# Performance work log

Measured on AMD Instinct MI355X. Metric: run time of the kernel, lower is better.

Reference implementation:

```python
import jax, jax.numpy as jnp
import numpy as np

D_MODEL = 1024
NUM_LAYERS = 4
VOCAB = 32000
NUM_HEADS = 8
HEAD_DIM = D_MODEL // NUM_HEADS
FFN_DIM = 2048
BATCH = 4
SEQ = 1024
LN_EPS = 1e-5
ROPE_THETA = 10000.0


def setup_inputs() -> dict:
    key = jax.random.key(0)
    ks = iter(jax.random.split(key, 32))
    std = 0.02
    L, D, H, Dh, F, V = NUM_LAYERS, D_MODEL, NUM_HEADS, HEAD_DIM, FFN_DIM, VOCAB
    inp = {
        "tokens": jax.random.randint(next(ks), (BATCH, SEQ), 0, V, dtype=jnp.int32),
        "emb": jax.random.normal(next(ks), (V, D), jnp.float32),
        # per-layer stacked params; Linear weights stored pre-transposed (in, out)
        "Wqkv": jax.random.normal(next(ks), (L, D, 3 * D), jnp.float32) * std,
        "bqkv": jnp.zeros((L, 3 * D), jnp.float32),
        "Wo": jax.random.normal(next(ks), (L, D, D), jnp.float32) * std,
        "bo": jnp.zeros((L, D), jnp.float32),
        "ln1_g": jnp.ones((L, D), jnp.float32),
        "ln1_b": jnp.zeros((L, D), jnp.float32),
        "ln2_g": jnp.ones((L, D), jnp.float32),
        "ln2_b": jnp.zeros((L, D), jnp.float32),
        "W1": jax.random.normal(next(ks), (L, D, F), jnp.float32) * std,
        "b1": jnp.zeros((L, F), jnp.float32),
        "W2": jax.random.normal(next(ks), (L, F, D), jnp.float32) * std,
        "b2": jnp.zeros((L, D), jnp.float32),
        "lnf_g": jnp.ones((D,), jnp.float32),
        "lnf_b": jnp.zeros((D,), jnp.float32),
        "Wout": jax.random.normal(next(ks), (D, V), jnp.float32) * std,
        "bout": jnp.zeros((V,), jnp.float32),
    }
    return inp


def _layernorm(x, g, b):
    mu = jnp.mean(x, -1, keepdims=True)
    var = jnp.mean(jnp.square(x - mu), -1, keepdims=True)
    return (x - mu) * jax.lax.rsqrt(var + LN_EPS) * g + b


def _rope_cos_sin(seq, dh, dtype):
    inv_freq = 1.0 / (ROPE_THETA ** (jnp.arange(0, dh, 2, dtype=jnp.float32) / dh))
    t = jnp.arange(seq, dtype=jnp.float32)
    freqs = jnp.outer(t, inv_freq)                      # [S, Dh/2]
    emb = jnp.concatenate([freqs, freqs], axis=-1)      # [S, Dh]
    return jnp.cos(emb).astype(dtype), jnp.sin(emb).astype(dtype)


def _rotate_half(x):
    x1, x2 = jnp.split(x, 2, axis=-1)
    return jnp.concatenate([-x2, x1], axis=-1)


def _apply_rope(x, cos, sin):
    # x: [B,S,H,Dh]; cos/sin: [S,Dh] -> broadcast over batch and heads
    return x * cos[None, :, None, :] + _rotate_half(x) * sin[None, :, None, :]


def reference(tokens, emb, Wqkv, bqkv, Wo, bo, ln1_g, ln1_b, ln2_g, ln2_b,
              W1, b1, W2, b2, lnf_g, lnf_b, Wout, bout):
    B, S = tokens.shape
    H, Dh = NUM_HEADS, HEAD_DIM
    x = emb[tokens]                                      # [B,S,D]
    cos, sin = _rope_cos_sin(S, Dh, x.dtype)
    causal = jnp.tril(jnp.ones((S, S), dtype=bool))      # True = keep
    scale = 1.0 / jnp.sqrt(jnp.asarray(Dh, x.dtype))

    def layer(xc, p):
        (wqkv, bq, wo, bo_, g1, b1_, g2, b2_, w1, bb1, w2, bb2) = p
        y = _layernorm(xc, g1, b1_)
        qkv = (y @ wqkv + bq).reshape(B, S, 3, H, Dh)
        q, k, v = qkv[:, :, 0], qkv[:, :, 1], qkv[:, :, 2]
        q = _apply_rope(q, cos, sin)
        k = _apply_rope(k, cos, sin)
        scores = jnp.einsum("bshd,bthd->bhst", q, k) * scale
        scores = jnp.where(causal[None, None], scores, -jnp.inf)
        attn = jax.nn.softmax(scores, axis=-1)
        ctx = jnp.einsum("bhst,bthd->bshd", attn, v).reshape(B, S, H * Dh)
        xc = xc + ctx @ wo + bo_
        z = _layernorm(xc, g2, b2_)
        ff = jax.nn.gelu(z @ w1 + bb1, approximate=False) @ w2 + bb2
        return xc + ff, None

    params = (Wqkv, bqkv, Wo, bo, ln1_g, ln1_b, ln2_g, ln2_b, W1, b1, W2, b2)
    x, _ = jax.lax.scan(layer, x, params)
    x = _layernorm(x, lnf_g, lnf_b)
    return x @ Wout + bout                                # [B,S,V]
```

## Files before the change

### kernel.cpp

```cpp
#include <hip/hip_runtime.h>
#include <hip/hip_bf16.h>
#include <math.h>


#define D_MODEL 1024
#define SEQ     1024
#define BATCH   4
#define NHEAD   8
#define HDIM    128
#define FFN     2048
#define NLAYER  4
#define VOCAB   32000
#define MROWS   (BATCH*SEQ)

typedef unsigned short ushort_t;
typedef __attribute__((ext_vector_type(8))) short s16x8;
typedef __attribute__((ext_vector_type(4))) float f32x4;

__device__ __forceinline__ ushort_t f2bf(float f) {
    union { float f; unsigned int u; } c; c.f = f;
    unsigned int u = c.u;
    unsigned int r = (u + 0x7FFFu + ((u >> 16) & 1u)) >> 16;
    return (ushort_t)r;
}
__device__ __forceinline__ float bf2f(ushort_t u) {
    union { unsigned int u; float f; } c; c.u = ((unsigned int)u) << 16; return c.f;
}

__device__ __forceinline__ void gload16(const void* g, void* l) {
    __builtin_amdgcn_global_load_lds(
        (const __attribute__((address_space(1))) unsigned int*)g,
        (__attribute__((address_space(3))) unsigned int*)l, 16, 0, 0);
}

__global__ __launch_bounds__(256) void embed_kernel(
    const int* __restrict__ tokens, const float* __restrict__ emb,
    float* __restrict__ X)
{
    int row = blockIdx.x;
    int t = tokens[row];
    const float4* src = (const float4*)(emb + (size_t)t * D_MODEL);
    float4* dst = (float4*)(X + (size_t)row * D_MODEL);
    dst[threadIdx.x] = src[threadIdx.x];
}

__global__ __launch_bounds__(256) void ln_kernel(
    const float* __restrict__ X, const float* __restrict__ g,
    const float* __restrict__ b, ushort_t* __restrict__ Y)
{
    __shared__ float red[8];
    int row = blockIdx.x;
    const float4* x4 = (const float4*)(X + (size_t)row * D_MODEL);
    float4 v = x4[threadIdx.x];
    float s  = v.x + v.y + v.z + v.w;
    float ss = v.x*v.x + v.y*v.y + v.z*v.z + v.w*v.w;
    #pragma unroll
    for (int o = 32; o > 0; o >>= 1) { s += __shfl_down(s, o); ss += __shfl_down(ss, o); }
    int wid = threadIdx.x >> 6;
    if ((threadIdx.x & 63) == 0) { red[wid] = s; red[wid + 4] = ss; }
    __syncthreads();
    float tot  = red[0] + red[1] + red[2] + red[3];
    float tot2 = red[4] + red[5] + red[6] + red[7];
    float mu  = tot * (1.0f / D_MODEL);
    float var = tot2 * (1.0f / D_MODEL) - mu * mu;
    float r = rsqrtf(var + 1e-5f);
    const float4* g4 = (const float4*)g;
    const float4* b4 = (const float4*)b;
    float4 gv = g4[threadIdx.x], bv = b4[threadIdx.x];
    ushort4 o;
    o.x = f2bf((v.x - mu) * r * gv.x + bv.x);
    o.y = f2bf((v.y - mu) * r * gv.y + bv.y);
    o.z = f2bf((v.z - mu) * r * gv.z + bv.z);
    o.w = f2bf((v.w - mu) * r * gv.w + bv.w);
    ((ushort4*)(Y + (size_t)row * D_MODEL))[threadIdx.x] = o;
}

__global__ __launch_bounds__(256) void wconv(
    const float* __restrict__ W, ushort_t* __restrict__ Wt, int K, int N)
{
    __shared__ float t[32][33];
    const float* Wl = W + (size_t)blockIdx.z * K * N;
    ushort_t* Wtl = Wt + (size_t)blockIdx.z * K * N;
    int k0 = blockIdx.y * 32, n0 = blockIdx.x * 32;
    int tid = threadIdx.x;
    int r = tid >> 3, c4 = (tid & 7) * 4;
    float4 v = *(const float4*)(Wl + (size_t)(k0 + r) * N + n0 + c4);
    t[r][c4+0] = v.x; t[r][c4+1] = v.y; t[r][c4+2] = v.z; t[r][c4+3] = v.w;
    __syncthreads();
    ushort4 o;
    o.x = f2bf(t[c4+0][r]); o.y = f2bf(t[c4+1][r]);
    o.z = f2bf(t[c4+2][r]); o.w = f2bf(t[c4+3][r]);
    *(ushort4*)(Wtl + (size_t)(n0 + r) * K + k0 + c4) = o;
}

__device__ __forceinline__ float gelu_exact(float x) {
    return 0.5f * x * (1.0f + erff(x * 0.70710678118654752f));
}

template<int ACT, int BETA, int OBF>
__global__ __launch_bounds__(256) void gemm_mfma(
    const ushort_t* __restrict__ A, const ushort_t* __restrict__ Bt,
    const float* __restrict__ bias, float* __restrict__ Cf,
    ushort_t* __restrict__ Cb, int M, int N, int K)
{
    __shared__ __align__(16) ushort_t As[128 * 32];
    __shared__ __align__(16) ushort_t Bs[128 * 32];
    int tid  = threadIdx.x;
    int lane = tid & 63, w = tid >> 6;
    int wr = w >> 1, wc = w & 1;
    int m0 = blockIdx.x * 128, n0 = blockIdx.y * 128;

    f32x4 acc[4][4] = {};

    const ushort_t* gA = A  + (size_t)(m0 + w * 32 + (lane >> 2)) * K + (lane & 3) * 8;
    const ushort_t* gB = Bt + (size_t)(n0 + w * 32 + (lane >> 2)) * K + (lane & 3) * 8;
    ushort_t* lA = As + w * 1024;
    ushort_t* lB = Bs + w * 1024;
    const size_t gstep16 = (size_t)16 * K;

    int lrow = lane & 15, kg = lane >> 4;
    const s16x8* pa = (const s16x8*)(As + (wr * 64 + lrow) * 32 + kg * 8);
    const s16x8* pb = (const s16x8*)(Bs + (wc * 64 + lrow) * 32 + kg * 8);

    for (int kt = 0; kt < K / 32; ++kt) {
        gload16(gA, lA);
        gload16(gA + gstep16, lA + 512);
        gload16(gB, lB);
        gload16(gB + gstep16, lB + 512);
        gA += 32; gB += 32;
        __syncthreads();
        s16x8 a[4], b[4];
        #pragma unroll
        for (int mi = 0; mi < 4; ++mi) a[mi] = pa[mi * 64];
        #pragma unroll
        for (int ni = 0; ni < 4; ++ni) b[ni] = pb[ni * 64];
        #pragma unroll
        for (int mi = 0; mi < 4; ++mi)
            #pragma unroll
            for (int ni = 0; ni < 4; ++ni)
                acc[mi][ni] = __builtin_amdgcn_mfma_f32_16x16x32_bf16(
                    a[mi], b[ni], acc[mi][ni], 0, 0, 0);
        __syncthreads();
    }

    #pragma unroll
    for (int mi = 0; mi < 4; ++mi) {
        int rbase = m0 + wr * 64 + mi * 16 + (lane >> 4) * 4;
        #pragma unroll
        for (int ni = 0; ni < 4; ++ni) {
            int col = n0 + wc * 64 + ni * 16 + (lane & 15);
            float bz = bias[col];
            f32x4 v = acc[mi][ni];
            #pragma unroll
            for (int j = 0; j < 4; ++j) {
                float x = v[j] + bz;
                if (ACT == 1) x = gelu_exact(x);
                size_t off = (size_t)(rbase + j) * N + col;
                if (OBF) {
                    Cb[off] = f2bf(x);
                } else {
                    if (BETA) x += Cf[off];
                    Cf[off] = x;
                }
            }
        }
    }
}

__global__ __launch_bounds__(512) void gemm_big(
    const ushort_t* __restrict__ A, const ushort_t* __restrict__ Bt,
    const float* __restrict__ bias, float* __restrict__ C,
    int M, int N, int K)
{
    __shared__ __align__(16) ushort_t As[2][256 * 64];
    __shared__ __align__(16) ushort_t Bs[2][256 * 64];
    int tid = threadIdx.x, lane = tid & 63, w = tid >> 6;
    int wm = w >> 2, wn = w & 3;
    int m0 = blockIdx.x * 256, n0 = blockIdx.y * 256;
    int lr = lane & 15, kg = lane >> 4;
    const int NKT = K / 64;

    f32x4 acc[8][4] = {};

    int srow = w * 8 + (lane >> 3);
    int scol = (((lane & 7) ^ ((lane >> 3) & 7))) * 8;

    int rsw = lr & 7;
    int ch0 = (kg    ) ^ rsw;
    int ch1 = (kg + 4) ^ rsw;

#define STAGE_A(db, ht, ktile) do { \
    const ushort_t* s_ = A + (size_t)(m0 + (ht) * 128 + srow) * K + (size_t)(ktile) * 64 + scol; \
    gload16(s_,                  &As[db][((ht) * 128 + w * 8) * 64]); \
    gload16(s_ + (size_t)64 * K, &As[db][((ht) * 128 + 64 + w * 8) * 64]); \
} while (0)
#define STAGE_B(db, ht, ktile) do { \
    const ushort_t* s_ = Bt + (size_t)(n0 + (ht) * 128 + srow) * K + (size_t)(ktile) * 64 + scol; \
    gload16(s_,                  &Bs[db][((ht) * 128 + w * 8) * 64]); \
    gload16(s_ + (size_t)64 * K, &Bs[db][((ht) * 128 + 64 + w * 8) * 64]); \
} while (0)
#define SBAR() do { __builtin_amdgcn_sched_barrier(0); \
    __builtin_amdgcn_s_barrier(); __builtin_amdgcn_sched_barrier(0); } while (0)

    STAGE_A(0, 0, 0); STAGE_A(0, 1, 0); STAGE_B(0, 0, 0); STAGE_B(0, 1, 0);
    STAGE_A(1, 0, 1);
    asm volatile("s_waitcnt vmcnt(2)" ::: "memory");
    SBAR();

    for (int kt = 0; kt < NKT; ++kt) {
        int d = kt & 1, dn = d ^ 1;
        const ushort_t* pa0 = &As[d][(wm * 128 + lr) * 64 + ch0 * 8];
        const ushort_t* pa1 = &As[d][(wm * 128 + lr) * 64 + ch1 * 8];
        const ushort_t* pb0 = &Bs[d][(wn * 64  + lr) * 64 + ch0 * 8];
        const ushort_t* pb1 = &Bs[d][(wn * 64  + lr) * 64 + ch1 * 8];
        s16x8 a03[4][2], a47[4][2], b01[2][2], b23[2][2];

        #pragma unroll
        for (int mi = 0; mi < 4; ++mi) {
            a03[mi][0] = *(const s16x8*)(pa0 + mi * 1024);
            a03[mi][1] = *(const s16x8*)(pa1 + mi * 1024);
        }
        #pragma unroll
        for (int ni = 0; ni < 2; ++ni) {
            b01[ni][0] = *(const s16x8*)(pb0 + ni * 1024);
            b01[ni][1] = *(const s16x8*)(pb1 + ni * 1024);
        }
        #pragma unroll
        for (int ni = 0; ni < 2; ++ni) {
            b23[ni][0] = *(const s16x8*)(pb0 + (2 + ni) * 1024);
            b23[ni][1] = *(const s16x8*)(pb1 + (2 + ni) * 1024);
        }
        #pragma unroll
        for (int mi = 0; mi < 4; ++mi) {
            a47[mi][0] = *(const s16x8*)(pa0 + (4 + mi) * 1024);
            a47[mi][1] = *(const s16x8*)(pa1 + (4 + mi) * 1024);
        }
        if (kt + 1 < NKT) STAGE_A(dn, 1, kt + 1);
        __builtin_amdgcn_sched_barrier(0);

        __builtin_amdgcn_s_setprio(1);
        #pragma unroll
        for (int mi = 0; mi < 4; ++mi)
            #pragma unroll
            for (int ni = 0; ni < 2; ++ni)
                #pragma unroll
                for (int kk = 0; kk < 2; ++kk)
                    acc[mi][ni] = __builtin_amdgcn_mfma_f32_16x16x32_bf16(
                        a03[mi][kk], b01[ni][kk], acc[mi][ni], 0, 0, 0);
        __builtin_amdgcn_s_setprio(0);
        __builtin_amdgcn_sched_barrier(0);
        if (kt + 1 < NKT) STAGE_B(dn, 0, kt + 1);
        __builtin_amdgcn_sched_barrier(0);

        __builtin_amdgcn_s_setprio(1);
        #pragma unroll
        for (int mi = 0; mi < 4; ++mi)
            #pragma unroll
            for (int ni = 0; ni < 2; ++ni)
                #pragma unroll
                for (int kk = 0; kk < 2; ++kk)
                    acc[mi][2 + ni] = __builtin_amdgcn_mfma_f32_16x16x32_bf16(
                        a03[mi][kk], b23[ni][kk], acc[mi][2 + ni], 0, 0, 0);
        __builtin_amdgcn_s_setprio(0);
        __builtin_amdgcn_sched_barrier(0);
        if (kt + 1 < NKT) STAGE_B(dn, 1, kt + 1);
        __builtin_amdgcn_sched_barrier(0);

        __builtin_amdgcn_s_setprio(1);
        #pragma unroll
        for (int mi = 0; mi < 4; ++mi)
            #pragma unroll
            for (int ni = 0; ni < 2; ++ni)
                #pragma unroll
                for (int kk = 0; kk < 2; ++kk)
                    acc[4 + mi][ni] = __builtin_amdgcn_mfma_f32_16x16x32_bf16(
                        a47[mi][kk], b01[ni][kk], acc[4 + mi][ni], 0, 0, 0);
        __builtin_amdgcn_s_setprio(0);

        asm volatile("s_waitcnt lgkmcnt(0)" ::: "memory");
        SBAR();
        if (kt + 2 < NKT) STAGE_A(d, 0, kt + 2);
        __builtin_amdgcn_sched_barrier(0);

        __builtin_amdgcn_s_setprio(1);
        #pragma unroll
        for (int mi = 0; mi < 4; ++mi)
            #pragma unroll
            for (int ni = 0; ni < 2; ++ni)
                #pragma unroll
                for (int kk = 0; kk < 2; ++kk)
                    acc[4 + mi][2 + ni] = __builtin_amdgcn_mfma_f32_16x16x32_bf16(
                        a47[mi][kk], b23[ni][kk], acc[4 + mi][2 + ni], 0, 0, 0);
        __builtin_amdgcn_s_setprio(0);

        if (kt + 2 < NKT) {
            asm volatile("s_waitcnt vmcnt(2)" ::: "memory");
        } else {
            asm volatile("s_waitcnt vmcnt(0)" ::: "memory");
        }
        SBAR();
    }
#undef STAGE_A
#undef STAGE_B
#undef SBAR

    #pragma unroll
    for (int mi = 0; mi < 8; ++mi) {
        int rbase = m0 + wm * 128 + mi * 16 + kg * 4;
        #pragma unroll
        for (int ni = 0; ni < 4; ++ni) {
            int col = n0 + wn * 64 + ni * 16 + lr;
            float bz = bias[col];
            f32x4 v = acc[mi][ni];
            #pragma unroll
            for (int j = 0; j < 4; ++j)
                C[(size_t)(rbase + j) * N + col] = v[j] + bz;
        }
    }
}

__global__ __launch_bounds__(64) void rope_table_kernel(float2* __restrict__ RT)
{
    int s = blockIdx.x, p = threadIdx.x;
    float inv = expf(-0.14391156831212788f * (float)p);
    float ang = (float)s * inv;
    float sn, c;
    sincosf(ang, &sn, &c);
    RT[s * 64 + p] = make_float2(c, sn);
}

__global__ __launch_bounds__(256) void ropeq_kernel(
    const ushort_t* __restrict__ QKVb, const float2* __restrict__ RT,
    ushort_t* __restrict__ Qb, ushort_t* __restrict__ Kb)
{
    int m = blockIdx.x;
    int b = m >> 10, s = m & (SEQ - 1);
    const ushort_t* rowbase = QKVb + (size_t)m * (3 * D_MODEL);
    const float2* t2 = RT + s * 64;
    int tid = threadIdx.x;
    int qk = tid >> 7;
    int rem = tid & 127;
    int hh = rem >> 4;
    int p4 = (rem & 15) * 4;
    const ushort_t* base = rowbase + qk * D_MODEL + hh * HDIM + p4;
    ushort4 lo = *(const ushort4*)base;
    ushort4 hi = *(const ushort4*)(base + 64);
    ushort_t lov[4] = {lo.x, lo.y, lo.z, lo.w};
    ushort_t hiv[4] = {hi.x, hi.y, hi.z, hi.w};
    ushort_t lor[4], hir[4];
    #pragma unroll
    for (int j = 0; j < 4; ++j) {
        float2 cs = t2[p4 + j];
        float x1 = bf2f(lov[j]), x2 = bf2f(hiv[j]);
        lor[j] = f2bf(x1 * cs.x - x2 * cs.y);
        hir[j] = f2bf(x2 * cs.x + x1 * cs.y);
    }
    ushort_t* dst = (qk ? Kb : Qb) + ((size_t)(b * NHEAD + hh) * SEQ + s) * HDIM + p4;
    *(ushort4*)dst        = make_ushort4(lor[0], lor[1], lor[2], lor[3]);
    *(ushort4*)(dst + 64) = make_ushort4(hir[0], hir[1], hir[2], hir[3]);
}

__global__ __launch_bounds__(256) void vtrans_kernel(
    const ushort_t* __restrict__ QKVb, ushort_t* __restrict__ Vt)
{
    __shared__ ushort_t tl[64][34];
    int s0 = blockIdx.x * 64;
    int d0 = blockIdx.y * 32;
    int b  = blockIdx.z;
    int tid = threadIdx.x;
    #pragma unroll
    for (int r = 0; r < 4; ++r) {
        int li = tid + r * 256;
        int row = li >> 4;
        int cp  = (li & 15) * 2;
        ushort2 v = *(const ushort2*)(QKVb + (size_t)(b * SEQ + s0 + row) * 3072
                                      + 2 * D_MODEL + d0 + cp);
        tl[row][cp]     = v.x;
        tl[row][cp + 1] = v.y;
    }
    __syncthreads();
    #pragma unroll
    for (int r = 0; r < 4; ++r) {
        int li = tid + r * 256;
        int drow = li >> 5;
        int sc   = (li & 31) * 2;
        ushort2 o;
        o.x = tl[sc][drow];
        o.y = tl[sc + 1][drow];
        *(ushort2*)(Vt + (size_t)(b * D_MODEL + d0 + drow) * SEQ + s0 + sc) = o;
    }
}

#define PSTR 72

__global__ __launch_bounds__(256) void attn_mfma(
    const ushort_t* __restrict__ Qb, const ushort_t* __restrict__ Kb,
    const ushort_t* __restrict__ Vt, ushort_t* __restrict__ Yb)
{
    __shared__ __align__(16) ushort_t Ks[64 * 136];
    __shared__ __align__(16) ushort_t Vts[128 * 72];
    __shared__ __align__(16) ushort_t Pl[4][16 * PSTR];
    int bid = blockIdx.x;
    int qt = bid & 15, h = (bid >> 4) & 7, b = bid >> 7;
    int q0 = qt * 64;
    int tid = threadIdx.x, lane = tid & 63, w = tid >> 6;
    int lr = lane & 15, g = lane >> 4;
    const float scale = 0.08838834764831845f;

    const ushort_t* Qbase = Qb + (size_t)((b * NHEAD + h) * SEQ) * HDIM;
    const ushort_t* Kbase = Kb + (size_t)((b * NHEAD + h) * SEQ) * HDIM;
    const ushort_t* Vbase = Vt + (size_t)(b * D_MODEL + h * HDIM) * SEQ;

    s16x8 aq[4];
    #pragma unroll
    for (int kc = 0; kc < 4; ++kc)
        aq[kc] = *(const s16x8*)(Qbase + (size_t)(q0 + w * 16 + lr) * HDIM + kc * 32 + g * 8);

    f32x4 acc_o[8] = {};
    float mx[4] = {-INFINITY, -INFINITY, -INFINITY, -INFINITY};
    float ls[4] = {};

    int ntiles = q0 / 64 + 1;
    for (int t = 0; t < ntiles; ++t) {
        int j0 = t * 64;
        __syncthreads();
        #pragma unroll
        for (int r = 0; r < 4; ++r) {
            int idx = tid + r * 256;
            int row = idx >> 4, c16 = idx & 15;
            *(s16x8*)&Ks[row * 136 + c16 * 8] =
                *(const s16x8*)(Kbase + (size_t)(j0 + row) * HDIM + c16 * 8);
        }
        #pragma unroll
        for (int r = 0; r < 4; ++r) {
            int idx = tid + r * 256;
            int row = idx >> 3, c8 = idx & 7;
            *(s16x8*)&Vts[row * 72 + c8 * 8] =
                *(const s16x8*)(Vbase + (size_t)row * SEQ + j0 + c8 * 8);
        }
        __syncthreads();

        f32x4 sa[4] = {};
        __builtin_amdgcn_s_setprio(1);
        #pragma unroll
        for (int nb = 0; nb < 4; ++nb)
            #pragma unroll
            for (int kc = 0; kc < 4; ++kc) {
                s16x8 bk = *(const s16x8*)&Ks[(nb * 16 + lr) * 136 + kc * 32 + g * 8];
                sa[nb] = __builtin_amdgcn_mfma_f32_16x16x32_bf16(aq[kc], bk, sa[nb], 0, 0, 0);
            }
        __builtin_amdgcn_s_setprio(0);

        bool diag = (j0 == q0);
        float pv[4][4];
        #pragma unroll
        for (int nb = 0; nb < 4; ++nb)
            #pragma unroll
            for (int j = 0; j < 4; ++j) {
                float v = sa[nb][j] * scale;
                if (diag) {
                    int kv = j0 + nb * 16 + lr;
                    int qq = q0 + w * 16 + g * 4 + j;
                    if (kv > qq) v = -INFINITY;
                }
                pv[nb][j] = v;
            }
        #pragma unroll
        for (int j = 0; j < 4; ++j) {
            float tm = fmaxf(fmaxf(pv[0][j], pv[1][j]), fmaxf(pv[2][j], pv[3][j]));
            #pragma unroll
            for (int o = 1; o < 16; o <<= 1) tm = fmaxf(tm, __shfl_xor(tm, o));
            float nm = fmaxf(mx[j], tm);
            float corr = expf(mx[j] - nm);
            float ts = 0.0f;
            #pragma unroll
            for (int nb = 0; nb < 4; ++nb) {
                float e = expf(pv[nb][j] - nm);
                pv[nb][j] = e;
                ts += e;
            }
            #pragma unroll
            for (int o = 1; o < 16; o <<= 1) ts += __shfl_xor(ts, o);
            ls[j] = ls[j] * corr + ts;
            mx[j] = nm;
            #pragma unroll
            for (int dn = 0; dn < 8; ++dn) acc_o[dn][j] *= corr;
        }
        #pragma unroll
        for (int nb = 0; nb < 4; ++nb)
            #pragma unroll
            for (int j = 0; j < 4; ++j)
                Pl[w][(g * 4 + j) * PSTR + nb * 16 + lr] = f2bf(pv[nb][j]);
        #pragma unroll
        for (int kk = 0; kk < 2; ++kk) {
            s16x8 pa = *(const s16x8*)&Pl[w][lr * PSTR + kk * 32 + g * 8];
            __builtin_amdgcn_s_setprio(1);
            #pragma unroll
            for (int dn = 0; dn < 8; ++dn) {
                s16x8 bv = *(const s16x8*)&Vts[(dn * 16 + lr) * 72 + kk * 32 + g * 8];
                acc_o[dn] = __builtin_amdgcn_mfma_f32_16x16x32_bf16(pa, bv, acc_o[dn], 0, 0, 0);
            }
            __builtin_amdgcn_s_setprio(0);
        }
    }

    float il[4];
    #pragma unroll
    for (int j = 0; j < 4; ++j) il[j] = 1.0f / ls[j];
    #pragma unroll
    for (int dn = 0; dn < 8; ++dn)
        #pragma unroll
        for (int j = 0; j < 4; ++j) {
            int q = q0 + w * 16 + g * 4 + j;
            Yb[(size_t)(b * SEQ + q) * D_MODEL + h * HDIM + dn * 16 + lr] =
                f2bf(acc_o[dn][j] * il[j]);
        }
}

extern "C" void kernel_launch(void* const* d_in, const int* in_sizes, int n_in,
                              void* d_out, int out_size, void* d_ws, size_t ws_size,
                              hipStream_t stream)
{
    const int*   tokens = (const int*)  d_in[0];
    const float* emb    = (const float*)d_in[1];
    const float* Wqkv   = (const float*)d_in[2];
    const float* bqkv   = (const float*)d_in[3];
    const float* Wo     = (const float*)d_in[4];
    const float* bo     = (const float*)d_in[5];
    const float* ln1_g  = (const float*)d_in[6];
    const float* ln1_b  = (const float*)d_in[7];
    const float* ln2_g  = (const float*)d_in[8];
    const float* ln2_b  = (const float*)d_in[9];
    const float* W1     = (const float*)d_in[10];
    const float* b1     = (const float*)d_in[11];
    const float* W2     = (const float*)d_in[12];
    const float* b2     = (const float*)d_in[13];
    const float* lnf_g  = (const float*)d_in[14];
    const float* lnf_b  = (const float*)d_in[15];
    const float* Wout   = (const float*)d_in[16];
    const float* bout   = (const float*)d_in[17];
    float* out = (float*)d_out;

    char* ws = (char*)d_ws;
    float*    X      = (float*)ws;
    ushort_t* Abuf   = (ushort_t*)(ws + 16777216);
    ushort_t* QKVb   = (ushort_t*)(ws + 25165824);
    ushort_t* Gbuf   = (ushort_t*)(ws + 25165824);
    ushort_t* Qbb    = (ushort_t*)(ws + 50331648);
    ushort_t* Kbb    = (ushort_t*)(ws + 58720256);
    ushort_t* Vtb    = (ushort_t*)(ws + 67108864);
    ushort_t* WqkvT  = (ushort_t*)(ws + 75497472);
    ushort_t* WoT    = (ushort_t*)(ws + 100663296);
    ushort_t* W1T    = (ushort_t*)(ws + 109051904);
    ushort_t* W2T    = (ushort_t*)(ws + 125829120);
    ushort_t* WoutT  = (ushort_t*)(ws + 142606336);
    float2*   RT     = (float2*)  (ws + 208142336);

    const int M = MROWS, Dm = D_MODEL, F = FFN, V = VOCAB;

    rope_table_kernel<<<SEQ, 64, 0, stream>>>(RT);

    wconv<<<dim3(3*Dm/32, Dm/32, NLAYER), 256, 0, stream>>>(Wqkv, WqkvT, Dm, 3*Dm);
    wconv<<<dim3(Dm/32,   Dm/32, NLAYER), 256, 0, stream>>>(Wo,   WoT,   Dm, Dm);
    wconv<<<dim3(F/32,    Dm/32, NLAYER), 256, 0, stream>>>(W1,   W1T,   Dm, F);
    wconv<<<dim3(Dm/32,   F/32,  NLAYER), 256, 0, stream>>>(W2,   W2T,   F,  Dm);
    wconv<<<dim3(V/32,    Dm/32, 1),      256, 0, stream>>>(Wout, WoutT, Dm, V);

    embed_kernel<<<MROWS, 256, 0, stream>>>(tokens, emb, X);

    for (int L = 0; L < NLAYER; ++L) {
        ln_kernel<<<MROWS, 256, 0, stream>>>(X, ln1_g + (size_t)L*Dm, ln1_b + (size_t)L*Dm, Abuf);
        gemm_mfma<0,0,1><<<dim3(M/128, 3*Dm/128), 256, 0, stream>>>(
            Abuf, WqkvT + (size_t)L*3*Dm*Dm, bqkv + (size_t)L*3*Dm, nullptr, QKVb, M, 3*Dm, Dm);
        ropeq_kernel<<<MROWS, 256, 0, stream>>>(QKVb, RT, Qbb, Kbb);
        vtrans_kernel<<<dim3(SEQ/64, Dm/32, BATCH), 256, 0, stream>>>(QKVb, Vtb);
        attn_mfma<<<BATCH*NHEAD*(SEQ/64), 256, 0, stream>>>(Qbb, Kbb, Vtb, Abuf);
        gemm_mfma<0,1,0><<<dim3(M/128, Dm/128), 256, 0, stream>>>(
            Abuf, WoT + (size_t)L*Dm*Dm, bo + (size_t)L*Dm, X, nullptr, M, Dm, Dm);
        ln_kernel<<<MROWS, 256, 0, stream>>>(X, ln2_g + (size_t)L*Dm, ln2_b + (size_t)L*Dm, Abuf);
        gemm_mfma<1,0,1><<<dim3(M/128, F/128), 256, 0, stream>>>(
            Abuf, W1T + (size_t)L*Dm*F, b1 + (size_t)L*F, nullptr, Gbuf, M, F, Dm);
        gemm_mfma<0,1,0><<<dim3(M/128, Dm/128), 256, 0, stream>>>(
            Gbuf, W2T + (size_t)L*F*Dm, b2 + (size_t)L*Dm, X, nullptr, M, Dm, F);
    }

    ln_kernel<<<MROWS, 256, 0, stream>>>(X, lnf_g, lnf_b, Abuf);
    gemm_big<<<dim3(M/256, V/256), 512, 0, stream>>>(
        Abuf, WoutT, bout, out, M, V, Dm);
}
```

Baseline: 1.516 ms.

## Double-buffer layer GEMMs with K=64 tiles, XOR-swizzled LDS and interleaved prefetch

```diff
diff --git a/kernel.cpp b/kernel.cpp
--- a/kernel.cpp
+++ b/kernel.cpp
@@ -31,6 +31,10 @@
     __builtin_amdgcn_global_load_lds(
         (const __attribute__((address_space(1))) unsigned int*)g,
         (__attribute__((address_space(3))) unsigned int*)l, 16, 0, 0);
+}
+
+__device__ __forceinline__ float gelu_exact(float x) {
+    return 0.5f * x * (1.0f + erff(x * 0.70710678118654752f));
 }
 
 __global__ __launch_bounds__(256) void embed_kernel(
@@ -93,62 +97,140 @@
     *(ushort4*)(Wtl + (size_t)(n0 + r) * K + k0 + c4) = o;
 }
 
-__device__ __forceinline__ float gelu_exact(float x) {
-    return 0.5f * x * (1.0f + erff(x * 0.70710678118654752f));
-}
-
 template<int ACT, int BETA, int OBF>
-__global__ __launch_bounds__(256) void gemm_mfma(
+__global__ __launch_bounds__(256) void gemm_mid(
     const ushort_t* __restrict__ A, const ushort_t* __restrict__ Bt,
     const float* __restrict__ bias, float* __restrict__ Cf,
     ushort_t* __restrict__ Cb, int M, int N, int K)
 {
-    __shared__ __align__(16) ushort_t As[128 * 32];
-    __shared__ __align__(16) ushort_t Bs[128 * 32];
-    int tid  = threadIdx.x;
-    int lane = tid & 63, w = tid >> 6;
-    int wr = w >> 1, wc = w & 1;
+    __shared__ __align__(16) ushort_t As[2][128 * 64];
+    __shared__ __align__(16) ushort_t Bs[2][128 * 64];
+    int tid = threadIdx.x, lane = tid & 63, w = tid >> 6;
+    int wm = w >> 1, wn = w & 1;
     int m0 = blockIdx.x * 128, n0 = blockIdx.y * 128;
+    int lr = lane & 15, kg = lane >> 4;
+    const int NKT = K / 64;
 
     f32x4 acc[4][4] = {};
 
-    const ushort_t* gA = A  + (size_t)(m0 + w * 32 + (lane >> 2)) * K + (lane & 3) * 8;
-    const ushort_t* gB = Bt + (size_t)(n0 + w * 32 + (lane >> 2)) * K + (lane & 3) * 8;
-    ushort_t* lA = As + w * 1024;
-    ushort_t* lB = Bs + w * 1024;
-    const size_t gstep16 = (size_t)16 * K;
-
-    int lrow = lane & 15, kg = lane >> 4;
-    const s16x8* pa = (const s16x8*)(As + (wr * 64 + lrow) * 32 + kg * 8);
-    const s16x8* pb = (const s16x8*)(Bs + (wc * 64 + lrow) * 32 + kg * 8);
-
-    for (int kt = 0; kt < K / 32; ++kt) {
-        gload16(gA, lA);
-        gload16(gA + gstep16, lA + 512);
-        gload16(gB, lB);
-        gload16(gB + gstep16, lB + 512);
-        gA += 32; gB += 32;
-        __syncthreads();
-        s16x8 a[4], b[4];
-        #pragma unroll
-        for (int mi = 0; mi < 4; ++mi) a[mi] = pa[mi * 64];
-        #pragma unroll
-        for (int ni = 0; ni < 4; ++ni) b[ni] = pb[ni * 64];
-        #pragma unroll
-        for (int mi = 0; mi < 4; ++mi)
-            #pragma unroll
-            for (int ni = 0; ni < 4; ++ni)
-                acc[mi][ni] = __builtin_amdgcn_mfma_f32_16x16x32_bf16(
-                    a[mi], b[ni], acc[mi][ni], 0, 0, 0);
-        __syncthreads();
-    }
+    int srow = w * 8 + (lane >> 3);
+    int scol = (((lane & 7) ^ ((lane >> 3) & 7))) * 8;
+
+    int rsw = lr & 7;
+    int ch0 = (kg    ) ^ rsw;
+    int ch1 = (kg + 4) ^ rsw;
+
+#define STAGE_A(db, ht, ktile) do { \
+    const ushort_t* s_ = A + (size_t)(m0 + (ht) * 64 + srow) * K + (size_t)(ktile) * 64 + scol; \
+    gload16(s_,                  &As[db][((ht) * 64 + w * 8) * 64]); \
+    gload16(s_ + (size_t)32 * K, &As[db][((ht) * 64 + 32 + w * 8) * 64]); \
+} while (0)
+#define STAGE_B(db, ht, ktile) do { \
+    const ushort_t* s_ = Bt + (size_t)(n0 + (ht) * 64 + srow) * K + (size_t)(ktile) * 64 + scol; \
+    gload16(s_,                  &Bs[db][((ht) * 64 + w * 8) * 64]); \
+    gload16(s_ + (size_t)32 * K, &Bs[db][((ht) * 64 + 32 + w * 8) * 64]); \
+} while (0)
+#define SBAR() do { __builtin_amdgcn_sched_barrier(0); \
+    __builtin_amdgcn_s_barrier(); __builtin_amdgcn_sched_barrier(0); } while (0)
+
+    STAGE_A(0, 0, 0); STAGE_A(0, 1, 0); STAGE_B(0, 0, 0); STAGE_B(0, 1, 0);
+    STAGE_A(1, 0, 1);
+    asm volatile("s_waitcnt vmcnt(2)" ::: "memory");
+    SBAR();
+
+    for (int kt = 0; kt < NKT; ++kt) {
+        int d = kt & 1, dn = d ^ 1;
+        const ushort_t* pa0 = &As[d][(wm * 64 + lr) * 64 + ch0 * 8];
+        const ushort_t* pa1 = &As[d][(wm * 64 + lr) * 64 + ch1 * 8];
+        const ushort_t* pb0 = &Bs[d][(wn * 64 + lr) * 64 + ch0 * 8];
+        const ushort_t* pb1 = &Bs[d][(wn * 64 + lr) * 64 + ch1 * 8];
+        s16x8 a[4][2], b[4][2];
+
+        #pragma unroll
+        for (int mi = 0; mi < 4; ++mi) {
+            a[mi][0] = *(const s16x8*)(pa0 + mi * 1024);
+            a[mi][1] = *(const s16x8*)(pa1 + mi * 1024);
+        }
+        #pragma unroll
+        for (int ni = 0; ni < 4; ++ni) {
+            b[ni][0] = *(const s16x8*)(pb0 + ni * 1024);
+            b[ni][1] = *(const s16x8*)(pb1 + ni * 1024);
+        }
+        if (kt + 1 < NKT) STAGE_A(dn, 1, kt + 1);
+        __builtin_amdgcn_sched_barrier(0);
+
+        __builtin_amdgcn_s_setprio(1);
+        #pragma unroll
+        for (int mi = 0; mi < 2; ++mi)
+            #pragma unroll
+            for (int ni = 0; ni < 2; ++ni)
+                #pragma unroll
+                for (int kk = 0; kk < 2; ++kk)
+                    acc[mi][ni] = __builtin_amdgcn_mfma_f32_16x16x32_bf16(
+                        a[mi][kk], b[ni][kk], acc[mi][ni], 0, 0, 0);
+        __builtin_amdgcn_s_setprio(0);
+        __builtin_amdgcn_sched_barrier(0);
+        if (kt + 1 < NKT) STAGE_B(dn, 0, kt + 1);
+        __builtin_amdgcn_sched_barrier(0);
+
+        __builtin_amdgcn_s_setprio(1);
+        #pragma unroll
+        for (int mi = 0; mi < 2; ++mi)
+            #pragma unroll
+            for (int ni = 2; ni < 4; ++ni)
+                #pragma unroll
+                for (int kk = 0; kk < 2; ++kk)
+                    acc[mi][ni] = __builtin_amdgcn_mfma_f32_16x16x32_bf16(
+                        a[mi][kk], b[ni][kk], acc[mi][ni], 0, 0, 0);
+        __builtin_amdgcn_s_setprio(0);
+        __builtin_amdgcn_sched_barrier(0);
+        if (kt + 1 < NKT) STAGE_B(dn, 1, kt + 1);
+        __builtin_amdgcn_sched_barrier(0);
+
+        __builtin_amdgcn_s_setprio(1);
+        #pragma unroll
+        for (int mi = 2; mi < 4; ++mi)
+            #pragma unroll
+            for (int ni = 0; ni < 2; ++ni)
+                #pragma unroll
+                for (int kk = 0; kk < 2; ++kk)
+                    acc[mi][ni] = __builtin_amdgcn_mfma_f32_16x16x32_bf16(
+                        a[mi][kk], b[ni][kk], acc[mi][ni], 0, 0, 0);
+        __builtin_amdgcn_s_setprio(0);
+
+        asm volatile("s_waitcnt lgkmcnt(0)" ::: "memory");
+        SBAR();
+        if (kt + 2 < NKT) STAGE_A(d, 0, kt + 2);
+        __builtin_amdgcn_sched_barrier(0);
+
+        __builtin_amdgcn_s_setprio(1);
+        #pragma unroll
+        for (int mi = 2; mi < 4; ++mi)
+            #pragma unroll
+            for (int ni = 2; ni < 4; ++ni)
+                #pragma unroll
+                for (int kk = 0; kk < 2; ++kk)
+                    acc[mi][ni] = __builtin_amdgcn_mfma_f32_16x16x32_bf16(
+                        a[mi][kk], b[ni][kk], acc[mi][ni], 0, 0, 0);
+        __builtin_amdgcn_s_setprio(0);
+
+        if (kt + 2 < NKT) {
+            asm volatile("s_waitcnt vmcnt(2)" ::: "memory");
+        } else {
+            asm volatile("s_waitcnt vmcnt(0)" ::: "memory");
+        }
+        SBAR();
+    }
+#undef STAGE_A
+#undef STAGE_B
+#undef SBAR
 
     #pragma unroll
     for (int mi = 0; mi < 4; ++mi) {
-        int rbase = m0 + wr * 64 + mi * 16 + (lane >> 4) * 4;
+        int rbase = m0 + wm * 64 + mi * 16 + kg * 4;
         #pragma unroll
         for (int ni = 0; ni < 4; ++ni) {
-            int col = n0 + wc * 64 + ni * 16 + (lane & 15);
+            int col = n0 + wn * 64 + ni * 16 + lr;
             float bz = bias[col];
             f32x4 v = acc[mi][ni];
             #pragma unroll
@@ -570,17 +652,17 @@
 
     for (int L = 0; L < NLAYER; ++L) {
         ln_kernel<<<MROWS, 256, 0, stream>>>(X, ln1_g + (size_t)L*Dm, ln1_b + (size_t)L*Dm, Abuf);
-        gemm_mfma<0,0,1><<<dim3(M/128, 3*Dm/128), 256, 0, stream>>>(
+        gemm_mid<0,0,1><<<dim3(M/128, 3*Dm/128), 256, 0, stream>>>(
             Abuf, WqkvT + (size_t)L*3*Dm*Dm, bqkv + (size_t)L*3*Dm, nullptr, QKVb, M, 3*Dm, Dm);
         ropeq_kernel<<<MROWS, 256, 0, stream>>>(QKVb, RT, Qbb, Kbb);
         vtrans_kernel<<<dim3(SEQ/64, Dm/32, BATCH), 256, 0, stream>>>(QKVb, Vtb);
         attn_mfma<<<BATCH*NHEAD*(SEQ/64), 256, 0, stream>>>(Qbb, Kbb, Vtb, Abuf);
-        gemm_mfma<0,1,0><<<dim3(M/128, Dm/128), 256, 0, stream>>>(
+        gemm_mid<0,1,0><<<dim3(M/128, Dm/128), 256, 0, stream>>>(
             Abuf, WoT + (size_t)L*Dm*Dm, bo + (size_t)L*Dm, X, nullptr, M, Dm, Dm);
         ln_kernel<<<MROWS, 256, 0, stream>>>(X, ln2_g + (size_t)L*Dm, ln2_b + (size_t)L*Dm, Abuf);
-        gemm_mfma<1,0,1><<<dim3(M/128, F/128), 256, 0, stream>>>(
+        gemm_mid<1,0,1><<<dim3(M/128, F/128), 256, 0, stream>>>(
             Abuf, W1T + (size_t)L*Dm*F, b1 + (size_t)L*F, nullptr, Gbuf, M, F, Dm);
-        gemm_mfma<0,1,0><<<dim3(M/128, Dm/128), 256, 0, stream>>>(
+        gemm_mid<0,1,0><<<dim3(M/128, Dm/128), 256, 0, stream>>>(
             Gbuf, W2T + (size_t)L*F*Dm, b2 + (size_t)L*Dm, X, nullptr, M, Dm, F);
     }
 
```

New measurement: 1.383 ms. -8.8%, faster.
